# Optimization experiments

Measured on AMD Instinct MI355X. Metric: run time of the kernel, lower is better.

The kernel has to match this reference:

```python
import jax, jax.numpy as jnp
import numpy as np

B, T, D, H, C = 8192, 2048, 1, 256, 10


def setup_inputs() -> dict:
    key = jax.random.key(0)
    ks = jax.random.split(key, 10)
    bound = float(np.sqrt(1.0 / H))
    u = lambda k, shape: jax.random.uniform(k, shape, jnp.float32, -bound, bound)
    return {
        "x": jax.random.normal(ks[0], (B, T), jnp.float32),
        "W_gx": u(ks[1], (D, H)), "W_gh": u(ks[2], (H, H)),
        "W_ix": u(ks[3], (D, H)), "W_ih": u(ks[4], (H, H)),
        "W_fx": u(ks[5], (D, H)), "W_fh": u(ks[6], (H, H)),
        "W_ox": u(ks[7], (D, H)), "W_oh": u(ks[8], (H, H)),
        "W_ph": u(ks[9], (H, C)),
        "b_g": jnp.zeros((1, H), jnp.float32),
        "b_i": jnp.zeros((1, H), jnp.float32),
        "b_f": jnp.ones((1, H), jnp.float32),   # forget-gate bias init = 1 as in source
        "b_o": jnp.zeros((1, H), jnp.float32),
        "b_p": jnp.zeros((1, C), jnp.float32),
    }


def reference(x, W_gx, W_gh, W_ix, W_ih, W_fx, W_fh, W_ox, W_oh, W_ph,
              b_g, b_i, b_f, b_o, b_p):
    # x: [B, T]; each timestep is a scalar feature (input_dim = 1).
    def step(carry, x_t):
        h, c = carry                      # [B, H] each
        xs = x_t[:, None]                 # [B, 1]
        g = jnp.tanh(xs @ W_gx + h @ W_gh + b_g)
        i = jax.nn.sigmoid(xs @ W_ix + h @ W_ih + b_i)
        f = jax.nn.sigmoid(xs @ W_fx + h @ W_fh + b_f)
        o = jax.nn.sigmoid(xs @ W_ox + h @ W_oh + b_o)
        c = g * i + c * f
        h = jnp.tanh(c) * o
        return (h, c), None

    h0 = jnp.zeros((x.shape[0], W_gh.shape[0]), x.dtype)
    c0 = jnp.zeros_like(h0)
    (h, _), _ = jax.lax.scan(step, (h0, c0), x.T)  # scan over time: [T, B]
    return h @ W_ph + b_p                          # [B, num_classes]
```

## Files before the change

kernel.cpp:

```cpp
#include <hip/hip_runtime.h>


#define TT 2048
#define HH 256
#define CC 10

typedef _Float16 half8 __attribute__((ext_vector_type(8)));
typedef float float4v __attribute__((ext_vector_type(4)));

#define WRES_OFF  0
#define RING_OFF  65536
#define RING_SLOT 16384
#define HF_OFF    131072
#define BW_OFF    147456
#define WW_OFF    151552
#define XS_OFF    155648
#define LDS_TOTAL 159744

__device__ __forceinline__ float frcp(float v)  { return __builtin_amdgcn_rcpf(v); }
__device__ __forceinline__ float fex2(float v)  { return __builtin_amdgcn_exp2f(v); }
__device__ __forceinline__ float fsig(float v)  { return frcp(1.0f + fex2(-1.442695040888963f * v)); }
__device__ __forceinline__ float ftanh(float v) { return 2.0f * frcp(1.0f + fex2(-2.885390081777927f * v)) - 1.0f; }

__device__ __forceinline__ void stream_issue(const void* g, void* l) {
    __builtin_amdgcn_global_load_lds((const __attribute__((address_space(1))) void*)g,
                                     (__attribute__((address_space(3))) void*)l, 16, 0, 0);
}
#define WAIT_VM4()     asm volatile("s_waitcnt vmcnt(4)" ::: "memory")
#define BARRIER_LGKM() asm volatile("s_waitcnt lgkmcnt(0)\n\ts_barrier" ::: "memory")

__global__ void pack_weights(const float* __restrict__ Wg, const float* __restrict__ Wi,
                             const float* __restrict__ Wf, const float* __restrict__ Wo,
                             _Float16* __restrict__ wsW) {
    int u = blockIdx.x * blockDim.x + threadIdx.x;
    int kk = u >> 12, rem = u & 4095;
    int s = rem >> 8, rem2 = rem & 255;
    int t = rem2 >> 6, lane = rem2 & 63;
    int q = lane >> 4, l15 = lane & 15;
    int jh = s * 16 + l15;
    const float* Wsrc = (t == 0) ? Wg : (t == 1) ? Wi : (t == 2) ? Wf : Wo;
    half8 v;
#pragma unroll
    for (int j = 0; j < 8; ++j) {
        int k = kk * 32 + q * 8 + j;
        v[j] = (_Float16)Wsrc[k * HH + jh];
    }
    ((half8*)wsW)[u] = v;
}

__attribute__((amdgpu_waves_per_eu(2, 2)))
__global__ void __launch_bounds__(512) lstm_main(
    const float* __restrict__ x, const _Float16* __restrict__ wsW,
    const float* __restrict__ Wgx, const float* __restrict__ Wix,
    const float* __restrict__ Wfx, const float* __restrict__ Wox,
    const float* __restrict__ bg, const float* __restrict__ bi,
    const float* __restrict__ bfp, const float* __restrict__ bo,
    const float* __restrict__ Wp, const float* __restrict__ bp,
    float* __restrict__ out)
{
    extern __shared__ char smem[];
    _Float16* hf  = (_Float16*)(smem + HF_OFF);
    float*    bwL = (float*)(smem + BW_OFF);
    float*    wwL = (float*)(smem + WW_OFF);
    float*    xsL = (float*)(smem + XS_OFF);

    const int tid  = threadIdx.x;
    const int wv   = tid >> 6;
    const int lane = tid & 63;
    const int q    = lane >> 4;
    const int l15  = lane & 15;
    const int s0   = wv * 2;
    const int b0   = blockIdx.x * 32;

    for (int i = tid; i < 8192; i += 512) hf[i] = (_Float16)0.f;
    {
        const uint4* src = (const uint4*)wsW;
        uint4* dst = (uint4*)(smem + WRES_OFF);
        for (int i = tid; i < 65536 / 16; i += 512) dst[i] = src[i];
    }
    {
        const float* bptr[4] = { bg, bi, bfp, bo };
        const float* wptr[4] = { Wgx, Wix, Wfx, Wox };
        for (int i = tid; i < 1024; i += 512) {
            int t = i >> 8, j = i & 255;
            bwL[i] = bptr[t][j];
            wwL[i] = wptr[t][j];
        }
    }
    __syncthreads();

    const char* wl = (const char*)wsW + s0 * 4096 + lane * 16;
    char* ringW = smem + RING_OFF + wv * 2048;
    const _Float16* ringR = (const _Float16*)(smem + RING_OFF) + wv * 1024 + lane * 8;

#pragma unroll
    for (int m = 0; m < 3; ++m) {
        const int kk = 1 + m, t = 0;
#pragma unroll
        for (int sp = 0; sp < 2; ++sp)
            stream_issue(wl + kk * 65536 + sp * 4096 + t * 1024,
                         ringW + m * RING_SLOT + sp * 1024);
    }

    float4v cst[2][2];
#pragma unroll
    for (int mt = 0; mt < 2; ++mt)
#pragma unroll
        for (int sp = 0; sp < 2; ++sp) cst[mt][sp] = (float4v){0.f, 0.f, 0.f, 0.f};

    const int wb = wv * 512 + ((l15 >> 3) * 16 + q * 4) * 8 + (l15 & 7);

#define AREAD(kkv, mtv) (*(const half8*)(hf + (mtv) * 4096 + (kkv) * 512 + lane * 8))

#pragma unroll 1
    for (int ts = 0; ts < TT; ++ts) {
        if ((ts & 31) == 0) {
            const int row = tid >> 4;
            const int c2  = (tid & 15) * 2;
            float2 xv2 = *(const float2*)&x[(b0 + row) * TT + ts + c2];
            *(float2*)&xsL[row * 32 + c2] = xv2;
            BARRIER_LGKM();
        }

        float xv[2][4];
#pragma unroll
        for (int mt = 0; mt < 2; ++mt)
#pragma unroll
            for (int r = 0; r < 4; ++r)
                xv[mt][r] = xsL[(mt * 16 + q * 4 + r) * 32 + (ts & 31)];

        float4v acc[2][2][4];
        half8 a0, a1;

#pragma unroll
        for (int t = 0; t < 4; ++t) {
#pragma unroll
            for (int sp = 0; sp < 2; ++sp) {
                const int jj = (s0 + sp) * 16 + l15;
                const float bb = bwL[t * 256 + jj];
                const float wx = wwL[t * 256 + jj];
#pragma unroll
                for (int mt = 0; mt < 2; ++mt)
#pragma unroll
                    for (int r = 0; r < 4; ++r)
                        acc[mt][sp][t][r] = bb + xv[mt][r] * wx;
            }
            a0 = AREAD(0, 0); a1 = AREAD(0, 1);
            {
                const char* lb = smem + WRES_OFF + s0 * 4096 + lane * 16;
#pragma unroll
                for (int sp = 0; sp < 2; ++sp) {
                    half8 bf = *(const half8*)(lb + sp * 4096 + t * 1024);
                    acc[0][sp][t] = __builtin_amdgcn_mfma_f32_16x16x32_f16(a0, bf, acc[0][sp][t], 0, 0, 0);
                    acc[1][sp][t] = __builtin_amdgcn_mfma_f32_16x16x32_f16(a1, bf, acc[1][sp][t], 0, 0, 0);
                }
            }
#pragma unroll
            for (int mm = 0; mm < 7; ++mm) {
                const int m = t * 7 + mm;
                const int kk = 1 + mm, slot = m & 3;
                a0 = AREAD(kk, 0); a1 = AREAD(kk, 1);
                WAIT_VM4();
                half8 bf0 = *(const half8*)(ringR + slot * 8192);
                half8 bf1 = *(const half8*)(ringR + slot * 8192 + 512);
                acc[0][0][t] = __builtin_amdgcn_mfma_f32_16x16x32_f16(a0, bf0, acc[0][0][t], 0, 0, 0);
                acc[1][0][t] = __builtin_amdgcn_mfma_f32_16x16x32_f16(a1, bf0, acc[1][0][t], 0, 0, 0);
                acc[0][1][t] = __builtin_amdgcn_mfma_f32_16x16x32_f16(a0, bf1, acc[0][1][t], 0, 0, 0);
                acc[1][1][t] = __builtin_amdgcn_mfma_f32_16x16x32_f16(a1, bf1, acc[1][1][t], 0, 0, 0);
                {
                    int n = m + 3; if (n >= 28) n -= 28;
                    const int tn = n / 7, kkn = 1 + (n % 7), sn = n & 3;
#pragma unroll
                    for (int sp = 0; sp < 2; ++sp)
                        stream_issue(wl + kkn * 65536 + sp * 4096 + tn * 1024,
                                     ringW + sn * RING_SLOT + sp * 1024);
                }
            }
#pragma unroll
            for (int sp = 0; sp < 2; ++sp)
#pragma unroll
                for (int mt = 0; mt < 2; ++mt)
#pragma unroll
                    for (int r = 0; r < 4; ++r)
                        acc[mt][sp][t][r] = (t == 0) ? ftanh(acc[mt][sp][t][r])
                                                     : fsig(acc[mt][sp][t][r]);
        }

        _Float16 hn[2][2][4];
#pragma unroll
        for (int mt = 0; mt < 2; ++mt)
#pragma unroll
            for (int sp = 0; sp < 2; ++sp)
#pragma unroll
                for (int r = 0; r < 4; ++r) {
                    float cn = acc[mt][sp][0][r] * acc[mt][sp][1][r]
                             + cst[mt][sp][r]   * acc[mt][sp][2][r];
                    cst[mt][sp][r] = cn;
                    hn[mt][sp][r] = (_Float16)(ftanh(cn) * acc[mt][sp][3][r]);
                }

        BARRIER_LGKM();
#pragma unroll
        for (int mt = 0; mt < 2; ++mt)
#pragma unroll
            for (int sp = 0; sp < 2; ++sp)
#pragma unroll
                for (int r = 0; r < 4; ++r)
                    hf[mt * 4096 + wb + sp * 256 + r * 8] = hn[mt][sp][r];
        BARRIER_LGKM();
    }

#pragma unroll
    for (int rr = 0; rr < 4; ++rr) {
        int b = wv * 4 + rr;
        int mt = b >> 4, m = b & 15;
        float hv[4];
#pragma unroll
        for (int a2 = 0; a2 < 4; ++a2) {
            int j = lane + a2 * 64;
            int idx = mt * 4096 + (j >> 5) * 512 + (((j >> 3) & 3) * 16 + m) * 8 + (j & 7);
            hv[a2] = (float)hf[idx];
        }
#pragma unroll
        for (int c = 0; c < CC; ++c) {
            float sacc = 0.f;
#pragma unroll
            for (int a2 = 0; a2 < 4; ++a2) sacc += hv[a2] * Wp[(lane + a2 * 64) * CC + c];
#pragma unroll
            for (int off = 32; off > 0; off >>= 1) sacc += __shfl_xor(sacc, off, 64);
            if (lane == 0) out[(b0 + b) * CC + c] = sacc + bp[c];
        }
    }
}

extern "C" void kernel_launch(void* const* d_in, const int* in_sizes, int n_in,
                              void* d_out, int out_size, void* d_ws, size_t ws_size,
                              hipStream_t stream) {
    (void)in_sizes; (void)n_in; (void)out_size; (void)ws_size;
    const float* x   = (const float*)d_in[0];
    const float* Wgx = (const float*)d_in[1];
    const float* Wgh = (const float*)d_in[2];
    const float* Wix = (const float*)d_in[3];
    const float* Wih = (const float*)d_in[4];
    const float* Wfx = (const float*)d_in[5];
    const float* Wfh = (const float*)d_in[6];
    const float* Wox = (const float*)d_in[7];
    const float* Woh = (const float*)d_in[8];
    const float* Wp  = (const float*)d_in[9];
    const float* bg  = (const float*)d_in[10];
    const float* bi  = (const float*)d_in[11];
    const float* bf  = (const float*)d_in[12];
    const float* bo  = (const float*)d_in[13];
    const float* bp  = (const float*)d_in[14];
    _Float16* wsW = (_Float16*)d_ws;

    pack_weights<<<128, 256, 0, stream>>>(Wgh, Wih, Wfh, Woh, wsW);

    hipFuncSetAttribute((const void*)lstm_main,
                        hipFuncAttributeMaxDynamicSharedMemorySize, LDS_TOTAL);
    lstm_main<<<256, 512, LDS_TOTAL, stream>>>(
        x, wsW, Wgx, Wix, Wfx, Wox, bg, bi, bf, bo, Wp, bp, (float*)d_out);
}
```

Measured before the change: 12.16 ms.

## Keep two K-chunks of recurrent weights in LDS and stream the rest through registers

Replaces the global-to-LDS ring buffer (global_load_lds with explicit vmcnt waits) with 128KB of resident LDS weights covering two K-chunks, streaming the remaining six chunks from global/L2 straight into a 4-deep register ring of half8 values. The MFMA loop is reordered to run kk-major over all four gates, and gate activations are interleaved into the tail of the streamed loop. This drops the LDS round-trip and manual waitcnt for streamed weights and raises the resident fraction, at the cost of more VGPRs and relying on compiler-inserted waits for register loads.

```diff
diff --git a/kernel.cpp b/kernel.cpp
--- a/kernel.cpp
+++ b/kernel.cpp
@@ -9,8 +9,6 @@
 typedef float float4v __attribute__((ext_vector_type(4)));
 
 #define WRES_OFF  0
-#define RING_OFF  65536
-#define RING_SLOT 16384
 #define HF_OFF    131072
 #define BW_OFF    147456
 #define WW_OFF    151552
@@ -22,11 +20,6 @@
 __device__ __forceinline__ float fsig(float v)  { return frcp(1.0f + fex2(-1.442695040888963f * v)); }
 __device__ __forceinline__ float ftanh(float v) { return 2.0f * frcp(1.0f + fex2(-2.885390081777927f * v)) - 1.0f; }
 
-__device__ __forceinline__ void stream_issue(const void* g, void* l) {
-    __builtin_amdgcn_global_load_lds((const __attribute__((address_space(1))) void*)g,
-                                     (__attribute__((address_space(3))) void*)l, 16, 0, 0);
-}
-#define WAIT_VM4()     asm volatile("s_waitcnt vmcnt(4)" ::: "memory")
 #define BARRIER_LGKM() asm volatile("s_waitcnt lgkmcnt(0)\n\ts_barrier" ::: "memory")
 
 __global__ void pack_weights(const float* __restrict__ Wg, const float* __restrict__ Wi,
@@ -47,6 +40,16 @@
     }
     ((half8*)wsW)[u] = v;
 }
+
+#define ACT_GATE(g)                                                            \
+    _Pragma("unroll")                                                          \
+    for (int sp_ = 0; sp_ < 2; ++sp_)                                          \
+        _Pragma("unroll")                                                      \
+        for (int mt_ = 0; mt_ < 2; ++mt_)                                      \
+            _Pragma("unroll")                                                  \
+            for (int r_ = 0; r_ < 4; ++r_)                                     \
+                acc[mt_][sp_][g][r_] = ((g) == 0) ? ftanh(acc[mt_][sp_][g][r_])\
+                                                  : fsig(acc[mt_][sp_][g][r_]);
 
 __attribute__((amdgpu_waves_per_eu(2, 2)))
 __global__ void __launch_bounds__(512) lstm_main(
@@ -76,7 +79,7 @@
     {
         const uint4* src = (const uint4*)wsW;
         uint4* dst = (uint4*)(smem + WRES_OFF);
-        for (int i = tid; i < 65536 / 16; i += 512) dst[i] = src[i];
+        for (int i = tid; i < 131072 / 16; i += 512) dst[i] = src[i];
     }
     {
         const float* bptr[4] = { bg, bi, bfp, bo };
@@ -90,17 +93,14 @@
     __syncthreads();
 
     const char* wl = (const char*)wsW + s0 * 4096 + lane * 16;
-    char* ringW = smem + RING_OFF + wv * 2048;
-    const _Float16* ringR = (const _Float16*)(smem + RING_OFF) + wv * 1024 + lane * 8;
-
-#pragma unroll
-    for (int m = 0; m < 3; ++m) {
-        const int kk = 1 + m, t = 0;
+    const char* lb = smem + WRES_OFF + s0 * 4096 + lane * 16;
+
+    half8 sbuf[4][2];
+#pragma unroll
+    for (int m = 0; m < 4; ++m)
 #pragma unroll
         for (int sp = 0; sp < 2; ++sp)
-            stream_issue(wl + kk * 65536 + sp * 4096 + t * 1024,
-                         ringW + m * RING_SLOT + sp * 1024);
-    }
+            sbuf[m][sp] = *(const half8*)(wl + 2 * 65536 + sp * 4096 + m * 1024);
 
     float4v cst[2][2];
 #pragma unroll
@@ -130,13 +130,11 @@
                 xv[mt][r] = xsL[(mt * 16 + q * 4 + r) * 32 + (ts & 31)];
 
         float4v acc[2][2][4];
-        half8 a0, a1;
-
-#pragma unroll
-        for (int t = 0; t < 4; ++t) {
-#pragma unroll
-            for (int sp = 0; sp < 2; ++sp) {
-                const int jj = (s0 + sp) * 16 + l15;
+#pragma unroll
+        for (int sp = 0; sp < 2; ++sp) {
+            const int jj = (s0 + sp) * 16 + l15;
+#pragma unroll
+            for (int t = 0; t < 4; ++t) {
                 const float bb = bwL[t * 256 + jj];
                 const float wx = wwL[t * 256 + jj];
 #pragma unroll
@@ -145,46 +143,44 @@
                     for (int r = 0; r < 4; ++r)
                         acc[mt][sp][t][r] = bb + xv[mt][r] * wx;
             }
-            a0 = AREAD(0, 0); a1 = AREAD(0, 1);
-            {
-                const char* lb = smem + WRES_OFF + s0 * 4096 + lane * 16;
-#pragma unroll
-                for (int sp = 0; sp < 2; ++sp) {
-                    half8 bf = *(const half8*)(lb + sp * 4096 + t * 1024);
+        }
+
+        half8 a0, a1;
+#pragma unroll
+        for (int kk = 0; kk < 2; ++kk) {
+            a0 = AREAD(kk, 0); a1 = AREAD(kk, 1);
+#pragma unroll
+            for (int sp = 0; sp < 2; ++sp)
+#pragma unroll
+                for (int t = 0; t < 4; ++t) {
+                    half8 bf = *(const half8*)(lb + kk * 65536 + sp * 4096 + t * 1024);
                     acc[0][sp][t] = __builtin_amdgcn_mfma_f32_16x16x32_f16(a0, bf, acc[0][sp][t], 0, 0, 0);
                     acc[1][sp][t] = __builtin_amdgcn_mfma_f32_16x16x32_f16(a1, bf, acc[1][sp][t], 0, 0, 0);
                 }
+        }
+
+#pragma unroll
+        for (int m = 0; m < 24; ++m) {
+            const int kk = 2 + (m >> 2), t = m & 3, sl = m & 3;
+            if (t == 0) { a0 = AREAD(kk, 0); a1 = AREAD(kk, 1); }
+            const half8 bf0 = sbuf[sl][0];
+            const half8 bf1 = sbuf[sl][1];
+            acc[0][0][t] = __builtin_amdgcn_mfma_f32_16x16x32_f16(a0, bf0, acc[0][0][t], 0, 0, 0);
+            acc[1][0][t] = __builtin_amdgcn_mfma_f32_16x16x32_f16(a1, bf0, acc[1][0][t], 0, 0, 0);
+            acc[0][1][t] = __builtin_amdgcn_mfma_f32_16x16x32_f16(a0, bf1, acc[0][1][t], 0, 0, 0);
+            acc[1][1][t] = __builtin_amdgcn_mfma_f32_16x16x32_f16(a1, bf1, acc[1][1][t], 0, 0, 0);
+            {
+                const int n  = (m < 20) ? (m + 4) : (m - 20);
+                const int nk = 2 + (n >> 2), nt = n & 3;
+#pragma unroll
+                for (int sp = 0; sp < 2; ++sp)
+                    sbuf[sl][sp] = *(const half8*)(wl + nk * 65536 + sp * 4096 + nt * 1024);
             }
-#pragma unroll
-            for (int mm = 0; mm < 7; ++mm) {
-                const int m = t * 7 + mm;
-                const int kk = 1 + mm, slot = m & 3;
-                a0 = AREAD(kk, 0); a1 = AREAD(kk, 1);
-                WAIT_VM4();
-                half8 bf0 = *(const half8*)(ringR + slot * 8192);
-                half8 bf1 = *(const half8*)(ringR + slot * 8192 + 512);
-                acc[0][0][t] = __builtin_amdgcn_mfma_f32_16x16x32_f16(a0, bf0, acc[0][0][t], 0, 0, 0);
-                acc[1][0][t] = __builtin_amdgcn_mfma_f32_16x16x32_f16(a1, bf0, acc[1][0][t], 0, 0, 0);
-                acc[0][1][t] = __builtin_amdgcn_mfma_f32_16x16x32_f16(a0, bf1, acc[0][1][t], 0, 0, 0);
-                acc[1][1][t] = __builtin_amdgcn_mfma_f32_16x16x32_f16(a1, bf1, acc[1][1][t], 0, 0, 0);
-                {
-                    int n = m + 3; if (n >= 28) n -= 28;
-                    const int tn = n / 7, kkn = 1 + (n % 7), sn = n & 3;
-#pragma unroll
-                    for (int sp = 0; sp < 2; ++sp)
-                        stream_issue(wl + kkn * 65536 + sp * 4096 + tn * 1024,
-                                     ringW + sn * RING_SLOT + sp * 1024);
-                }
-            }
-#pragma unroll
-            for (int sp = 0; sp < 2; ++sp)
-#pragma unroll
-                for (int mt = 0; mt < 2; ++mt)
-#pragma unroll
-                    for (int r = 0; r < 4; ++r)
-                        acc[mt][sp][t][r] = (t == 0) ? ftanh(acc[mt][sp][t][r])
-                                                     : fsig(acc[mt][sp][t][r]);
-        }
+            if (m == 20) { ACT_GATE(0) }
+            if (m == 21) { ACT_GATE(1) }
+            if (m == 22) { ACT_GATE(2) }
+        }
+        ACT_GATE(3)
 
         _Float16 hn[2][2][4];
 #pragma unroll
```

Result: faster. 11.56 ms (median of 2 runs) (-4.9%).
